# Kernel tuning notes

Hardware: AMD Instinct MI355X
Metric: run time of the kernel (lower is better)

## Reference

```python
import jax, jax.numpy as jnp
import numpy as np

EPS = 1e-5

def _bn(x, gamma, beta):
    # BatchNorm1d forward (batch statistics, biased variance) over node dim
    mu = x.mean(axis=0)
    var = x.var(axis=0)
    return gamma * (x - mu) * jax.lax.rsqrt(var + EPS) + beta

def _gcn_conv(x, W, b, src, dst, n):
    # PyG GCNConv: h = x @ W; symmetric norm with self-loops; scatter-add to dst
    h = x @ W                                   # [N, out]
    ones = jnp.ones(src.shape, dtype=h.dtype)
    deg = jax.ops.segment_sum(ones, dst, num_segments=n) + 1.0  # +1 self-loop
    dinv = jax.lax.rsqrt(deg)                   # deg >= 1 always
    norm = dinv[src] * dinv[dst]                # [E]
    agg = jax.ops.segment_sum(h[src] * norm[:, None], dst, num_segments=n)
    agg = agg + h * (dinv * dinv)[:, None]      # self-loop contribution
    return agg + b

def setup_inputs() -> dict:
    key = jax.random.key(0)
    ks = jax.random.split(key, 10)
    N, E = 100000, 1600000
    Din, Dh, Dout = 256, 128, 128
    e_prev = jax.random.normal(ks[0], (N, Din), dtype=jnp.float32)
    edge_index = jax.random.randint(ks[1], (2, E), 0, N, dtype=jnp.int64)
    proj_W = jax.random.normal(ks[2], (Din, Din), dtype=jnp.float32) * 0.02
    proj_b = jnp.zeros((Din,), dtype=jnp.float32)
    W1 = jax.random.normal(ks[3], (Din, Dh), dtype=jnp.float32) * 0.05
    b1 = jnp.zeros((Dh,), dtype=jnp.float32)
    gamma1 = jnp.ones((Dh,), dtype=jnp.float32)
    beta1 = jnp.zeros((Dh,), dtype=jnp.float32)
    W2 = jax.random.normal(ks[4], (Dh, Dout), dtype=jnp.float32) * 0.05
    b2 = jnp.zeros((Dout,), dtype=jnp.float32)
    gamma2 = jnp.ones((Dout,), dtype=jnp.float32)
    beta2 = jnp.zeros((Dout,), dtype=jnp.float32)
    return {"e_prev": e_prev, "edge_index": edge_index,
            "proj_W": proj_W, "proj_b": proj_b,
            "W1": W1, "b1": b1, "gamma1": gamma1, "beta1": beta1,
            "W2": W2, "b2": b2, "gamma2": gamma2, "beta2": beta2}

def reference(e_prev, edge_index, proj_W, proj_b, W1, b1, gamma1, beta1, W2, b2, gamma2, beta2):
    n = e_prev.shape[0]
    src, dst = edge_index[0], edge_index[1]
    # input_projection (input_dim != hidden_dim branch)
    x = e_prev @ proj_W + proj_b
    x = _gcn_conv(x, W1, b1, src, dst, n)
    x = _bn(x, gamma1, beta1)
    x = jax.nn.relu(x)
    # dropout(0.2) is identity in eval mode
    x = _gcn_conv(x, W2, b2, src, dst, n)
    x = _bn(x, gamma2, beta2)
    return x
```

## Files before the change

kernel.cpp:

```cpp
#include <hip/hip_runtime.h>
#include <hip/hip_bf16.h>
#include <math.h>

#define BN_EPS 1e-5f
#define CAP 6144
#define MAXB 512

typedef __attribute__((ext_vector_type(8))) short short8;
typedef __attribute__((ext_vector_type(4))) float floatx4;

__device__ inline float4 ntload4(const float* p) {
    floatx4 v = __builtin_nontemporal_load((const floatx4*)p);
    return make_float4(v.x, v.y, v.z, v.w);
}

__global__ __launch_bounds__(128) void prep_kernel(
    const float* __restrict__ PW, const float* __restrict__ W1,
    const float* __restrict__ pb, const float* __restrict__ W2,
    __hip_bfloat16* __restrict__ Wf1, __hip_bfloat16* __restrict__ Wf2,
    float* __restrict__ bc, int* __restrict__ bcursor, int nb)
{
    int bid = blockIdx.x;
    int tid = threadIdx.x;
    if (bid < 256) {
        int k = bid, c = tid;
        float acc = 0.f;
        for (int kk = 0; kk < 256; ++kk) acc = fmaf(PW[k * 256 + kk], W1[kk * 128 + c], acc);
        int kc = k >> 5, r5 = k & 31, qq = r5 >> 3, j = r5 & 7;
        int ct = c >> 4, l16 = c & 15;
        int lane = qq * 16 + l16;
        Wf1[(((kc * 8 + ct) * 64) + lane) * 8 + j] = __float2bfloat16(acc);
    } else if (bid == 256) {
        int c = tid;
        float acc = 0.f;
        for (int k = 0; k < 256; ++k) acc = fmaf(pb[k], W1[k * 128 + c], acc);
        bc[c] = acc;
    } else if (bid < 385) {
        int t = (bid - 257) * 128 + tid;
        int j    = t & 7;
        int lane = (t >> 3) & 63;
        int ct   = (t >> 9) & 7;
        int kc   = t >> 12;
        int k = kc * 32 + ((lane >> 4) & 3) * 8 + j;
        int c = ct * 16 + (lane & 15);
        Wf2[t] = __float2bfloat16(W2[k * 128 + c]);
    } else {
        int i = (bid - 385) * 128 + tid;
        if (i < nb) bcursor[i] = i * CAP;
        if (bid == 385 && tid < 2) bcursor[nb + 8 + tid] = 0;
    }
}

__global__ __launch_bounds__(256) void bucket_kernel(
    const int* __restrict__ src, const int* __restrict__ dst,
    int* __restrict__ bcursor, unsigned* __restrict__ buck, int E, int nb)
{
    __shared__ int h[MAXB], resv[MAXB], cur[MAXB];
    for (int t = threadIdx.x; t < nb; t += 256) { h[t] = 0; cur[t] = 0; }
    __syncthreads();
    int per = (E + gridDim.x - 1) / gridDim.x;
    int e0 = blockIdx.x * per;
    int e1 = min(e0 + per, E);
    for (int e = e0 + threadIdx.x; e < e1; e += 256) {
        int d = __builtin_nontemporal_load(&dst[e]);
        atomicAdd(&h[d >> 8], 1);
    }
    __syncthreads();
    for (int t = threadIdx.x; t < nb; t += 256) {
        int c = h[t];
        if (c > 0) resv[t] = atomicAdd(&bcursor[t], c);
    }
    __syncthreads();
    for (int e = e0 + threadIdx.x; e < e1; e += 256) {
        int d = __builtin_nontemporal_load(&dst[e]);
        int s = __builtin_nontemporal_load(&src[e]);
        int b = d >> 8;
        int pos = resv[b] + atomicAdd(&cur[b], 1);
        buck[pos] = ((unsigned)(d & 255) << 17) | (unsigned)s;
    }
}

__global__ __launch_bounds__(256) void csr_kernel(
    const unsigned* __restrict__ buck, const int* __restrict__ bcursor,
    int* __restrict__ cnt, int* __restrict__ rowptr, float* __restrict__ dinv,
    int* __restrict__ ssrc, int N)
{
    __shared__ int h[256], sc[256], lcur[256], redu[256];
    int b = blockIdx.x;
    int t = threadIdx.x;
    int part = 0;
    for (int i = t; i < b; i += 256) part += bcursor[i] - i * CAP;
    redu[t] = part;
    h[t] = 0;
    __syncthreads();
    for (int off = 128; off > 0; off >>= 1) {
        if (t < off) redu[t] += redu[t + off];
        __syncthreads();
    }
    int cb = redu[0];

    int base = b * CAP;
    int nB = bcursor[b] - base;
    for (int i = t; i < nB; i += 256) {
        unsigned v = buck[base + i];
        atomicAdd(&h[v >> 17], 1);
    }
    __syncthreads();
    int myc = h[t];
    sc[t] = myc;
    __syncthreads();
    for (int off = 1; off < 256; off <<= 1) {
        int x = (t >= off) ? sc[t - off] : 0;
        __syncthreads();
        sc[t] += x;
        __syncthreads();
    }
    int ex = sc[t] - myc;
    lcur[t] = ex;
    int node = b * 256 + t;
    if (node < N) {
        cnt[node]    = myc;
        rowptr[node] = cb + ex;
        dinv[node]   = rsqrtf((float)myc + 1.0f);
    }
    __syncthreads();
    for (int i = t; i < nB; i += 256) {
        unsigned v = buck[base + i];
        int dloc = v >> 17;
        int pos = cb + atomicAdd(&lcur[dloc], 1);
        ssrc[pos] = (int)(v & 0x1FFFFu);
    }
}

__device__ inline short8 cvt8(float4 a, float4 b) {
    __hip_bfloat162 p0 = __float22bfloat162_rn(make_float2(a.x, a.y));
    __hip_bfloat162 p1 = __float22bfloat162_rn(make_float2(a.z, a.w));
    __hip_bfloat162 p2 = __float22bfloat162_rn(make_float2(b.x, b.y));
    __hip_bfloat162 p3 = __float22bfloat162_rn(make_float2(b.z, b.w));
    union { short8 s; __hip_bfloat162 h[4]; } u;
    u.h[0] = p0; u.h[1] = p1; u.h[2] = p2; u.h[3] = p3;
    return u.s;
}

template <int K, bool BN>
__global__ __launch_bounds__(256) void mfma_gemm(
    const float* __restrict__ X, const short* __restrict__ Wf,
    const float* __restrict__ bias, const float* __restrict__ dinv,
    const float* __restrict__ scale, const float* __restrict__ shift,
    __hip_bfloat16* __restrict__ Hs, int N)
{
    const int wave = threadIdx.x >> 6;
    const int lane = threadIdx.x & 63;
    const int l16  = lane & 15;
    const int q    = lane >> 4;
    const int r0   = blockIdx.x * 128 + wave * 32;

    const int ra0 = min(r0 + l16, N - 1);
    const int ra1 = min(r0 + 16 + l16, N - 1);
    const float* pA0 = X + (size_t)ra0 * K + q * 8;
    const float* pA1 = X + (size_t)ra1 * K + q * 8;
    const short8* WF = (const short8*)Wf;

    floatx4 acc[2][8];
#pragma unroll
    for (int rt = 0; rt < 2; ++rt)
#pragma unroll
        for (int ct = 0; ct < 8; ++ct) { acc[rt][ct][0] = 0.f; acc[rt][ct][1] = 0.f; acc[rt][ct][2] = 0.f; acc[rt][ct][3] = 0.f; }

#pragma unroll
    for (int kc = 0; kc < K / 32; ++kc) {
        short8 b[8];
#pragma unroll
        for (int ct = 0; ct < 8; ++ct) b[ct] = WF[(kc * 8 + ct) * 64 + lane];

        float4 x00 = ntload4(pA0 + kc * 32);
        float4 x01 = ntload4(pA0 + kc * 32 + 4);
        float4 x10 = ntload4(pA1 + kc * 32);
        float4 x11 = ntload4(pA1 + kc * 32 + 4);
        if (BN) {
            float4 sc0 = *(const float4*)(scale + kc * 32 + q * 8);
            float4 sc1 = *(const float4*)(scale + kc * 32 + q * 8 + 4);
            float4 sh0 = *(const float4*)(shift + kc * 32 + q * 8);
            float4 sh1 = *(const float4*)(shift + kc * 32 + q * 8 + 4);
            x00.x = fmaxf(fmaf(x00.x, sc0.x, sh0.x), 0.f);
            x00.y = fmaxf(fmaf(x00.y, sc0.y, sh0.y), 0.f);
            x00.z = fmaxf(fmaf(x00.z, sc0.z, sh0.z), 0.f);
            x00.w = fmaxf(fmaf(x00.w, sc0.w, sh0.w), 0.f);
            x01.x = fmaxf(fmaf(x01.x, sc1.x, sh1.x), 0.f);
            x01.y = fmaxf(fmaf(x01.y, sc1.y, sh1.y), 0.f);
            x01.z = fmaxf(fmaf(x01.z, sc1.z, sh1.z), 0.f);
            x01.w = fmaxf(fmaf(x01.w, sc1.w, sh1.w), 0.f);
            x10.x = fmaxf(fmaf(x10.x, sc0.x, sh0.x), 0.f);
            x10.y = fmaxf(fmaf(x10.y, sc0.y, sh0.y), 0.f);
            x10.z = fmaxf(fmaf(x10.z, sc0.z, sh0.z), 0.f);
            x10.w = fmaxf(fmaf(x10.w, sc0.w, sh0.w), 0.f);
            x11.x = fmaxf(fmaf(x11.x, sc1.x, sh1.x), 0.f);
            x11.y = fmaxf(fmaf(x11.y, sc1.y, sh1.y), 0.f);
            x11.z = fmaxf(fmaf(x11.z, sc1.z, sh1.z), 0.f);
            x11.w = fmaxf(fmaf(x11.w, sc1.w, sh1.w), 0.f);
        }
        short8 a0 = cvt8(x00, x01);
        short8 a1 = cvt8(x10, x11);
#pragma unroll
        for (int ct = 0; ct < 8; ++ct) {
            acc[0][ct] = __builtin_amdgcn_mfma_f32_16x16x32_bf16(a0, b[ct], acc[0][ct], 0, 0, 0);
            acc[1][ct] = __builtin_amdgcn_mfma_f32_16x16x32_bf16(a1, b[ct], acc[1][ct], 0, 0, 0);
        }
    }

    float bb[8];
#pragma unroll
    for (int ct = 0; ct < 8; ++ct) bb[ct] = bias ? bias[ct * 16 + l16] : 0.f;

#pragma unroll
    for (int rt = 0; rt < 2; ++rt) {
        int rbase = r0 + rt * 16 + q * 4;
        float dv[4];
#pragma unroll
        for (int i = 0; i < 4; ++i) dv[i] = dinv[min(rbase + i, N - 1)];
#pragma unroll
        for (int ct = 0; ct < 8; ++ct) {
#pragma unroll
            for (int i = 0; i < 4; ++i) {
                int row = rbase + i;
                if (row < N)
                    Hs[(size_t)row * 128 + ct * 16 + l16] =
                        __float2bfloat16((acc[rt][ct][i] + bb[ct]) * dv[i]);
            }
        }
    }
}

__device__ inline void accrow(uint4 u, float* a) {
    a[0] += __uint_as_float(u.x << 16);
    a[1] += __uint_as_float(u.x & 0xffff0000u);
    a[2] += __uint_as_float(u.y << 16);
    a[3] += __uint_as_float(u.y & 0xffff0000u);
    a[4] += __uint_as_float(u.z << 16);
    a[5] += __uint_as_float(u.z & 0xffff0000u);
    a[6] += __uint_as_float(u.w << 16);
    a[7] += __uint_as_float(u.w & 0xffff0000u);
}

__global__ __launch_bounds__(256) void agg_gather_kernel(
    const uint4* __restrict__ Hq, const int* __restrict__ rowptr,
    const int* __restrict__ cnt, const int* __restrict__ ssrc,
    const float* __restrict__ dinv, const float* __restrict__ bias,
    float* __restrict__ Out, int node0, int N)
{
    int node = node0 + blockIdx.x * 4 + (threadIdx.x >> 6);
    if (node >= N) return;
    int lane = threadIdx.x & 63;
    int q    = lane >> 4;
    int l16  = lane & 15;

    float a0[8] = {0,0,0,0,0,0,0,0};
    float a1[8] = {0,0,0,0,0,0,0,0};
    float a2[8] = {0,0,0,0,0,0,0,0};
    float a3[8] = {0,0,0,0,0,0,0,0};

    if (q == 0) accrow(Hq[(size_t)node * 16 + l16], a0);

    int start = rowptr[node];
    int num   = cnt[node];
    int j = 0;
    for (; j + 16 <= num; j += 16) {
        int e = start + j + q;
        int s0 = ssrc[e];
        int s1 = ssrc[e + 4];
        int s2 = ssrc[e + 8];
        int s3 = ssrc[e + 12];
        uint4 u0 = Hq[(size_t)s0 * 16 + l16];
        uint4 u1 = Hq[(size_t)s1 * 16 + l16];
        uint4 u2 = Hq[(size_t)s2 * 16 + l16];
        uint4 u3 = Hq[(size_t)s3 * 16 + l16];
        accrow(u0, a0);
        accrow(u1, a1);
        accrow(u2, a2);
        accrow(u3, a3);
    }
    for (; j + 4 <= num; j += 4) {
        int s = ssrc[start + j + q];
        accrow(Hq[(size_t)s * 16 + l16], a0);
    }
    int rem = num - j;
    if (q < rem) {
        int s = ssrc[start + j + q];
        accrow(Hq[(size_t)s * 16 + l16], a1);
    }

#pragma unroll
    for (int i = 0; i < 8; ++i) {
        float v = a0[i] + a1[i] + a2[i] + a3[i];
        v += __shfl_xor(v, 16, 64);
        v += __shfl_xor(v, 32, 64);
        a0[i] = v;
    }

    if (q == 0) {
        float di = dinv[node];
        const float4* B4 = (const float4*)bias;
        float4 bb0 = B4[l16 * 2];
        float4 bb1 = B4[l16 * 2 + 1];
        float4 o0, o1;
        o0.x = fmaf(a0[0], di, bb0.x);
        o0.y = fmaf(a0[1], di, bb0.y);
        o0.z = fmaf(a0[2], di, bb0.z);
        o0.w = fmaf(a0[3], di, bb0.w);
        o1.x = fmaf(a0[4], di, bb1.x);
        o1.y = fmaf(a0[5], di, bb1.y);
        o1.z = fmaf(a0[6], di, bb1.z);
        o1.w = fmaf(a0[7], di, bb1.w);
        float4* O4 = (float4*)(Out + (size_t)node * 128 + l16 * 8);
        O4[0] = o0;
        O4[1] = o1;
    }
}

__global__ __launch_bounds__(256) void bn_stats_kernel(
    const float* __restrict__ A, float* __restrict__ partS, float* __restrict__ partQ,
    int N, int R,
    const float* __restrict__ gamma, const float* __restrict__ beta,
    float* __restrict__ scale, float* __restrict__ shift, int* __restrict__ ctr)
{
    int col4   = threadIdx.x & 31;
    int rowoff = threadIdx.x >> 5;
    int r0 = blockIdx.x * R;
    int r1 = min(r0 + R, N);
    float4 s = make_float4(0.f, 0.f, 0.f, 0.f);
    float4 qq = make_float4(0.f, 0.f, 0.f, 0.f);
#pragma unroll 4
    for (int r = r0 + rowoff; r < r1; r += 8) {
        float4 v = *(const float4*)&A[(size_t)r * 128 + col4 * 4];
        s.x += v.x; s.y += v.y; s.z += v.z; s.w += v.w;
        qq.x = fmaf(v.x, v.x, qq.x);
        qq.y = fmaf(v.y, v.y, qq.y);
        qq.z = fmaf(v.z, v.z, qq.z);
        qq.w = fmaf(v.w, v.w, qq.w);
    }
    __shared__ float4 ls[256], lq[256];
    ls[threadIdx.x] = s;
    lq[threadIdx.x] = qq;
    __syncthreads();
    if (threadIdx.x < 32) {
        float4 ts = ls[threadIdx.x], tq = lq[threadIdx.x];
#pragma unroll
        for (int k = 1; k < 8; ++k) {
            float4 xs = ls[k * 32 + threadIdx.x];
            float4 xq = lq[k * 32 + threadIdx.x];
            ts.x += xs.x; ts.y += xs.y; ts.z += xs.z; ts.w += xs.w;
            tq.x += xq.x; tq.y += xq.y; tq.z += xq.z; tq.w += xq.w;
        }
        *(float4*)&partS[(size_t)blockIdx.x * 128 + threadIdx.x * 4] = ts;
        *(float4*)&partQ[(size_t)blockIdx.x * 128 + threadIdx.x * 4] = tq;
    }
    __syncthreads();
    __shared__ int amLast;
    if (threadIdx.x == 0) {
        __threadfence();
        amLast = (atomicAdd(ctr, 1) == (int)gridDim.x - 1);
    }
    __syncthreads();
    if (!amLast) return;
    __threadfence();
    int c = threadIdx.x & 127;
    int h = threadIdx.x >> 7;
    float fs = 0.f, fq = 0.f;
    for (int b = h * 128; b < h * 128 + 128; ++b) {
        fs += partS[(size_t)b * 128 + c];
        fq += partQ[(size_t)b * 128 + c];
    }
    __shared__ float rs_[256], rq_[256];
    rs_[threadIdx.x] = fs;
    rq_[threadIdx.x] = fq;
    __syncthreads();
    if (threadIdx.x < 128) {
        float S = rs_[threadIdx.x] + rs_[threadIdx.x + 128];
        float Q = rq_[threadIdx.x] + rq_[threadIdx.x + 128];
        float m = S / (float)N;
        float v = Q / (float)N - m * m;
        float rs = rsqrtf(v + BN_EPS);
        float sc = gamma[c] * rs;
        scale[c] = sc;
        shift[c] = fmaf(-m, sc, beta[c]);
    }
}

__global__ void bn_apply_kernel(float* __restrict__ A, const float* __restrict__ scale,
                                const float* __restrict__ shift, int N) {
    int i = blockIdx.x * blockDim.x + threadIdx.x;
    if (i >= N * 32) return;
    int c4 = i & 31;
    float4 v  = ((float4*)A)[i];
    float4 sc = ((const float4*)scale)[c4];
    float4 sh = ((const float4*)shift)[c4];
    v.x = fmaf(v.x, sc.x, sh.x);
    v.y = fmaf(v.y, sc.y, sh.y);
    v.z = fmaf(v.z, sc.z, sh.z);
    v.w = fmaf(v.w, sc.w, sh.w);
    ((float4*)A)[i] = v;
}

extern "C" void kernel_launch(void* const* d_in, const int* in_sizes, int n_in,
                              void* d_out, int out_size, void* d_ws, size_t ws_size,
                              hipStream_t stream) {
    const float* e_prev = (const float*)d_in[0];
    const int*   edges  = (const int*)d_in[1];
    const float* proj_W = (const float*)d_in[2];
    const float* proj_b = (const float*)d_in[3];
    const float* W1     = (const float*)d_in[4];
    const float* b1     = (const float*)d_in[5];
    const float* gamma1 = (const float*)d_in[6];
    const float* beta1  = (const float*)d_in[7];
    const float* W2     = (const float*)d_in[8];
    const float* b2     = (const float*)d_in[9];
    const float* gamma2 = (const float*)d_in[10];
    const float* beta2  = (const float*)d_in[11];
    float* out = (float*)d_out;

    const int N = in_sizes[0] / 256;
    const int E = in_sizes[1] / 2;
    const int* src = edges;
    const int* dst = edges + E;
    const int nb = (N + 255) >> 8;
    const int R = (N + 255) / 256;

    char* p = (char*)d_ws;
    const size_t NH = (size_t)N * 128;
    __hip_bfloat16* Hs = (__hip_bfloat16*)p;  p += NH * 2;
    unsigned* buck  = (unsigned*)p; p += (size_t)nb * CAP * 4;
    int* ssrc   = (int*)p;  p += (size_t)E * 4;
    int* cnt    = (int*)p;  p += (size_t)N * 4;
    int* rowptr = (int*)p;  p += (size_t)N * 4;
    float* dinv = (float*)p; p += (size_t)N * 4;
    int* bcursor = (int*)p; p += (size_t)(nb + 16) * 4;
    float* bc   = (float*)p; p += 128 * 4;
    float* stats = (float*)p; p += 1536 * 4;
    float* partS = (float*)p; p += 256 * 128 * 4;
    float* partQ = (float*)p; p += 256 * 128 * 4;
    __hip_bfloat16* Wf1 = (__hip_bfloat16*)p; p += 256 * 128 * 2;
    __hip_bfloat16* Wf2 = (__hip_bfloat16*)p; p += 128 * 128 * 2;
    float* scale1 = stats, *shift1 = stats + 128;
    float* scale2 = stats + 256, *shift2 = stats + 384;
    int* ctr1 = bcursor + nb + 8;
    int* ctr2 = bcursor + nb + 9;

    prep_kernel<<<389, 128, 0, stream>>>(proj_W, W1, proj_b, W2, Wf1, Wf2, bc, bcursor, nb);
    bucket_kernel<<<512, 256, 0, stream>>>(src, dst, bcursor, buck, E, nb);
    csr_kernel<<<nb, 256, 0, stream>>>(buck, bcursor, cnt, rowptr, dinv, ssrc, N);

    const int gemm_grid = (N + 127) / 128;
    const int Nh = ((N / 2) + 3) & ~3;
    const int g1 = Nh / 4;
    const int g2 = (N - Nh + 3) / 4;

    mfma_gemm<256, false><<<gemm_grid, 256, 0, stream>>>(
        e_prev, (const short*)Wf1, bc, dinv, nullptr, nullptr, Hs, N);
    agg_gather_kernel<<<g1, 256, 0, stream>>>(
        (const uint4*)Hs, rowptr, cnt, ssrc, dinv, b1, out, 0, N);
    agg_gather_kernel<<<g2, 256, 0, stream>>>(
        (const uint4*)Hs, rowptr, cnt, ssrc, dinv, b1, out, Nh, N);
    bn_stats_kernel<<<256, 256, 0, stream>>>(out, partS, partQ, N, R,
                                             gamma1, beta1, scale1, shift1, ctr1);

    mfma_gemm<128, true><<<gemm_grid, 256, 0, stream>>>(
        out, (const short*)Wf2, nullptr, dinv, scale1, shift1, Hs, N);
    agg_gather_kernel<<<g1, 256, 0, stream>>>(
        (const uint4*)Hs, rowptr, cnt, ssrc, dinv, b2, out, 0, N);
    agg_gather_kernel<<<g2, 256, 0, stream>>>(
        (const uint4*)Hs, rowptr, cnt, ssrc, dinv, b2, out, Nh, N);
    bn_stats_kernel<<<256, 256, 0, stream>>>(out, partS, partQ, N, R,
                                             gamma2, beta2, scale2, shift2, ctr2);
    bn_apply_kernel<<<(N * 32 + 255) / 256, 256, 0, stream>>>(out, scale2, shift2, N);
}
```

Before: 571.9 us.

## Fuse GEMM1 with bucketing, move dinv scaling into gather, fuse final BN

Several separate changes. GEMM1 now runs in one launch alongside edge bucketing, so the dense work overlaps the scatter. Because GEMM1 no longer needs dinv from the CSR pass, the source-side dinv scaling moves into the gather loop as an extra per-edge load. The split two-launch aggregation becomes a single launch, and the final BN stats and apply are merged into one kernel that uses a grid-wide spin barrier. The prep matmul loops also get four independent accumulators; the costs are extra dinv gathers per edge and a spin barrier that assumes all 256 blocks are resident at once.

New measurement: 596.5 us. 4.3% more time.

```diff
diff --git a/kernel.cpp b/kernel.cpp
--- a/kernel.cpp
+++ b/kernel.cpp
@@ -24,17 +24,28 @@
     int tid = threadIdx.x;
     if (bid < 256) {
         int k = bid, c = tid;
-        float acc = 0.f;
-        for (int kk = 0; kk < 256; ++kk) acc = fmaf(PW[k * 256 + kk], W1[kk * 128 + c], acc);
+        float a0 = 0.f, a1 = 0.f, a2 = 0.f, a3 = 0.f;
+        for (int kk = 0; kk < 256; kk += 4) {
+            a0 = fmaf(PW[k * 256 + kk],     W1[(kk)     * 128 + c], a0);
+            a1 = fmaf(PW[k * 256 + kk + 1], W1[(kk + 1) * 128 + c], a1);
+            a2 = fmaf(PW[k * 256 + kk + 2], W1[(kk + 2) * 128 + c], a2);
+            a3 = fmaf(PW[k * 256 + kk + 3], W1[(kk + 3) * 128 + c], a3);
+        }
+        float acc = (a0 + a1) + (a2 + a3);
         int kc = k >> 5, r5 = k & 31, qq = r5 >> 3, j = r5 & 7;
         int ct = c >> 4, l16 = c & 15;
         int lane = qq * 16 + l16;
         Wf1[(((kc * 8 + ct) * 64) + lane) * 8 + j] = __float2bfloat16(acc);
     } else if (bid == 256) {
         int c = tid;
-        float acc = 0.f;
-        for (int k = 0; k < 256; ++k) acc = fmaf(pb[k], W1[k * 128 + c], acc);
-        bc[c] = acc;
+        float a0 = 0.f, a1 = 0.f, a2 = 0.f, a3 = 0.f;
+        for (int k = 0; k < 256; k += 4) {
+            a0 = fmaf(pb[k],     W1[(k)     * 128 + c], a0);
+            a1 = fmaf(pb[k + 1], W1[(k + 1) * 128 + c], a1);
+            a2 = fmaf(pb[k + 2], W1[(k + 2) * 128 + c], a2);
+            a3 = fmaf(pb[k + 3], W1[(k + 3) * 128 + c], a3);
+        }
+        bc[c] = (a0 + a1) + (a2 + a3);
     } else if (bid < 385) {
         int t = (bid - 257) * 128 + tid;
         int j    = t & 7;
@@ -51,15 +62,16 @@
     }
 }
 
-__global__ __launch_bounds__(256) void bucket_kernel(
+__device__ void bucket_body(
     const int* __restrict__ src, const int* __restrict__ dst,
-    int* __restrict__ bcursor, unsigned* __restrict__ buck, int E, int nb)
+    int* __restrict__ bcursor, unsigned* __restrict__ buck,
+    int E, int nb, int nblocks, int bid)
 {
     __shared__ int h[MAXB], resv[MAXB], cur[MAXB];
     for (int t = threadIdx.x; t < nb; t += 256) { h[t] = 0; cur[t] = 0; }
     __syncthreads();
-    int per = (E + gridDim.x - 1) / gridDim.x;
-    int e0 = blockIdx.x * per;
+    int per = (E + nblocks - 1) / nblocks;
+    int e0 = bid * per;
     int e1 = min(e0 + per, E);
     for (int e = e0 + threadIdx.x; e < e1; e += 256) {
         int d = __builtin_nontemporal_load(&dst[e]);
@@ -143,9 +155,10 @@
 }
 
 template <int K, bool BN>
-__global__ __launch_bounds__(256) void mfma_gemm(
+__device__ void gemm_body(
+    int bid,
     const float* __restrict__ X, const short* __restrict__ Wf,
-    const float* __restrict__ bias, const float* __restrict__ dinv,
+    const float* __restrict__ bias,
     const float* __restrict__ scale, const float* __restrict__ shift,
     __hip_bfloat16* __restrict__ Hs, int N)
 {
@@ -153,7 +166,7 @@
     const int lane = threadIdx.x & 63;
     const int l16  = lane & 15;
     const int q    = lane >> 4;
-    const int r0   = blockIdx.x * 128 + wave * 32;
+    const int r0   = bid * 128 + wave * 32;
 
     const int ra0 = min(r0 + l16, N - 1);
     const int ra1 = min(r0 + 16 + l16, N - 1);
@@ -215,9 +228,6 @@
 #pragma unroll
     for (int rt = 0; rt < 2; ++rt) {
         int rbase = r0 + rt * 16 + q * 4;
-        float dv[4];
-#pragma unroll
-        for (int i = 0; i < 4; ++i) dv[i] = dinv[min(rbase + i, N - 1)];
 #pragma unroll
         for (int ct = 0; ct < 8; ++ct) {
 #pragma unroll
@@ -225,30 +235,53 @@
                 int row = rbase + i;
                 if (row < N)
                     Hs[(size_t)row * 128 + ct * 16 + l16] =
-                        __float2bfloat16((acc[rt][ct][i] + bb[ct]) * dv[i]);
+                        __float2bfloat16(acc[rt][ct][i] + bb[ct]);
             }
         }
     }
 }
 
-__device__ inline void accrow(uint4 u, float* a) {
-    a[0] += __uint_as_float(u.x << 16);
-    a[1] += __uint_as_float(u.x & 0xffff0000u);
-    a[2] += __uint_as_float(u.y << 16);
-    a[3] += __uint_as_float(u.y & 0xffff0000u);
-    a[4] += __uint_as_float(u.z << 16);
-    a[5] += __uint_as_float(u.z & 0xffff0000u);
-    a[6] += __uint_as_float(u.w << 16);
-    a[7] += __uint_as_float(u.w & 0xffff0000u);
+__global__ __launch_bounds__(256) void gemm1_bucket_kernel(
+    const float* __restrict__ X, const short* __restrict__ Wf,
+    const float* __restrict__ bias,
+    __hip_bfloat16* __restrict__ Hs, int N, int gemmGrid,
+    const int* __restrict__ src, const int* __restrict__ dst,
+    int* __restrict__ bcursor, unsigned* __restrict__ buck, int E, int nb,
+    int bucketGrid)
+{
+    if ((int)blockIdx.x < gemmGrid)
+        gemm_body<256, false>(blockIdx.x, X, Wf, bias, nullptr, nullptr, Hs, N);
+    else
+        bucket_body(src, dst, bcursor, buck, E, nb, bucketGrid,
+                    (int)blockIdx.x - gemmGrid);
+}
+
+__global__ __launch_bounds__(256) void mfma_gemm2_kernel(
+    const float* __restrict__ X, const short* __restrict__ Wf,
+    const float* __restrict__ scale, const float* __restrict__ shift,
+    __hip_bfloat16* __restrict__ Hs, int N)
+{
+    gemm_body<128, true>(blockIdx.x, X, Wf, nullptr, scale, shift, Hs, N);
+}
+
+__device__ inline void accrow(uint4 u, float d, float* a) {
+    a[0] = fmaf(__uint_as_float(u.x << 16),         d, a[0]);
+    a[1] = fmaf(__uint_as_float(u.x & 0xffff0000u), d, a[1]);
+    a[2] = fmaf(__uint_as_float(u.y << 16),         d, a[2]);
+    a[3] = fmaf(__uint_as_float(u.y & 0xffff0000u), d, a[3]);
+    a[4] = fmaf(__uint_as_float(u.z << 16),         d, a[4]);
+    a[5] = fmaf(__uint_as_float(u.z & 0xffff0000u), d, a[5]);
+    a[6] = fmaf(__uint_as_float(u.w << 16),         d, a[6]);
+    a[7] = fmaf(__uint_as_float(u.w & 0xffff0000u), d, a[7]);
 }
 
 __global__ __launch_bounds__(256) void agg_gather_kernel(
     const uint4* __restrict__ Hq, const int* __restrict__ rowptr,
     const int* __restrict__ cnt, const int* __restrict__ ssrc,
     const float* __restrict__ dinv, const float* __restrict__ bias,
-    float* __restrict__ Out, int node0, int N)
-{
-    int node = node0 + blockIdx.x * 4 + (threadIdx.x >> 6);
+    float* __restrict__ Out, int N)
+{
+    int node = blockIdx.x * 4 + (threadIdx.x >> 6);
     if (node >= N) return;
     int lane = threadIdx.x & 63;
     int q    = lane >> 4;
@@ -259,7 +292,8 @@
     float a2[8] = {0,0,0,0,0,0,0,0};
     float a3[8] = {0,0,0,0,0,0,0,0};
 
-    if (q == 0) accrow(Hq[(size_t)node * 16 + l16], a0);
+    float di = dinv[node];
+    if (q == 0) accrow(Hq[(size_t)node * 16 + l16], di, a0);
 
     int start = rowptr[node];
     int num   = cnt[node];
@@ -270,23 +304,27 @@
         int s1 = ssrc[e + 4];
         int s2 = ssrc[e + 8];
         int s3 = ssrc[e + 12];
+        float d0 = dinv[s0];
+        float d1 = dinv[s1];
+        float d2 = dinv[s2];
+        float d3 = dinv[s3];
         uint4 u0 = Hq[(size_t)s0 * 16 + l16];
         uint4 u1 = Hq[(size_t)s1 * 16 + l16];
         uint4 u2 = Hq[(size_t)s2 * 16 + l16];
         uint4 u3 = Hq[(size_t)s3 * 16 + l16];
-        accrow(u0, a0);
-        accrow(u1, a1);
-        accrow(u2, a2);
-        accrow(u3, a3);
+        accrow(u0, d0, a0);
+        accrow(u1, d1, a1);
+        accrow(u2, d2, a2);
+        accrow(u3, d3, a3);
     }
     for (; j + 4 <= num; j += 4) {
         int s = ssrc[start + j + q];
-        accrow(Hq[(size_t)s * 16 + l16], a0);
+        accrow(Hq[(size_t)s * 16 + l16], dinv[s], a0);
     }
     int rem = num - j;
     if (q < rem) {
         int s = ssrc[start + j + q];
-        accrow(Hq[(size_t)s * 16 + l16], a1);
+        accrow(Hq[(size_t)s * 16 + l16], dinv[s], a1);
     }
 
 #pragma unroll
@@ -298,7 +336,6 @@
     }
 
     if (q == 0) {
-        float di = dinv[node];
         const float4* B4 = (const float4*)bias;
         float4 bb0 = B4[l16 * 2];
         float4 bb1 = B4[l16 * 2 + 1];
@@ -386,19 +423,83 @@
     }
 }
 
-__global__ void bn_apply_kernel(float* __restrict__ A, const float* __restrict__ scale,
-                                const float* __restrict__ shift, int N) {
-    int i = blockIdx.x * blockDim.x + threadIdx.x;
-    if (i >= N * 32) return;
-    int c4 = i & 31;
-    float4 v  = ((float4*)A)[i];
-    float4 sc = ((const float4*)scale)[c4];
-    float4 sh = ((const float4*)shift)[c4];
-    v.x = fmaf(v.x, sc.x, sh.x);
-    v.y = fmaf(v.y, sc.y, sh.y);
-    v.z = fmaf(v.z, sc.z, sh.z);
-    v.w = fmaf(v.w, sc.w, sh.w);
-    ((float4*)A)[i] = v;
+__global__ __launch_bounds__(256) void bn_stats_apply_kernel(
+    float* __restrict__ A, float* __restrict__ partS, float* __restrict__ partQ,
+    int N, int R,
+    const float* __restrict__ gamma, const float* __restrict__ beta,
+    int* __restrict__ ctr)
+{
+    int col4   = threadIdx.x & 31;
+    int rowoff = threadIdx.x >> 5;
+    int r0 = blockIdx.x * R;
+    int r1 = min(r0 + R, N);
+    float4 s = make_float4(0.f, 0.f, 0.f, 0.f);
+    float4 qq = make_float4(0.f, 0.f, 0.f, 0.f);
+#pragma unroll 4
+    for (int r = r0 + rowoff; r < r1; r += 8) {
+        float4 v = *(const float4*)&A[(size_t)r * 128 + col4 * 4];
+        s.x += v.x; s.y += v.y; s.z += v.z; s.w += v.w;
+        qq.x = fmaf(v.x, v.x, qq.x);
+        qq.y = fmaf(v.y, v.y, qq.y);
+        qq.z = fmaf(v.z, v.z, qq.z);
+        qq.w = fmaf(v.w, v.w, qq.w);
+    }
+    __shared__ float4 ls[256], lq[256];
+    ls[threadIdx.x] = s;
+    lq[threadIdx.x] = qq;
+    __syncthreads();
+    if (threadIdx.x < 32) {
+        float4 ts = ls[threadIdx.x], tq = lq[threadIdx.x];
+#pragma unroll
+        for (int k = 1; k < 8; ++k) {
+            float4 xs = ls[k * 32 + threadIdx.x];
+            float4 xq = lq[k * 32 + threadIdx.x];
+            ts.x += xs.x; ts.y += xs.y; ts.z += xs.z; ts.w += xs.w;
+            tq.x += xq.x; tq.y += xq.y; tq.z += xq.z; tq.w += xq.w;
+        }
+        *(float4*)&partS[(size_t)blockIdx.x * 128 + threadIdx.x * 4] = ts;
+        *(float4*)&partQ[(size_t)blockIdx.x * 128 + threadIdx.x * 4] = tq;
+    }
+    __syncthreads();
+    if (threadIdx.x == 0) {
+        __threadfence();
+        atomicAdd(ctr, 1);
+        while (atomicAdd(ctr, 0) < (int)gridDim.x) { }
+    }
+    __syncthreads();
+    __threadfence();
+    int c = threadIdx.x & 127;
+    int h = threadIdx.x >> 7;
+    float fs = 0.f, fq = 0.f;
+    for (int b = h * 128; b < h * 128 + 128; ++b) {
+        fs += partS[(size_t)b * 128 + c];
+        fq += partQ[(size_t)b * 128 + c];
+    }
+    __shared__ float rs_[256], rq_[256];
+    __shared__ float s_sc[128], s_sh[128];
+    rs_[threadIdx.x] = fs;
+    rq_[threadIdx.x] = fq;
+    __syncthreads();
+    if (threadIdx.x < 128) {
+        float S = rs_[threadIdx.x] + rs_[threadIdx.x + 128];
+        float Q = rq_[threadIdx.x] + rq_[threadIdx.x + 128];
+        float m = S / (float)N;
+        float v = Q / (float)N - m * m;
+        float rs = rsqrtf(v + BN_EPS);
+        float sc = gamma[threadIdx.x] * rs;
+        s_sc[threadIdx.x] = sc;
+        s_sh[threadIdx.x] = fmaf(-m, sc, beta[threadIdx.x]);
+    }
+    __syncthreads();
+    for (int r = r0 + rowoff; r < r1; r += 8) {
+        float4* pv = (float4*)&A[(size_t)r * 128 + col4 * 4];
+        float4 v = *pv;
+        v.x = fmaf(v.x, s_sc[col4 * 4 + 0], s_sh[col4 * 4 + 0]);
+        v.y = fmaf(v.y, s_sc[col4 * 4 + 1], s_sh[col4 * 4 + 1]);
+        v.z = fmaf(v.z, s_sc[col4 * 4 + 2], s_sh[col4 * 4 + 2]);
+        v.w = fmaf(v.w, s_sc[col4 * 4 + 3], s_sh[col4 * 4 + 3]);
+        *pv = v;
+    }
 }
 
 extern "C" void kernel_launch(void* const* d_in, const int* in_sizes, int n_in,
@@ -441,35 +542,25 @@
     __hip_bfloat16* Wf1 = (__hip_bfloat16*)p; p += 256 * 128 * 2;
     __hip_bfloat16* Wf2 = (__hip_bfloat16*)p; p += 128 * 128 * 2;
     float* scale1 = stats, *shift1 = stats + 128;
-    float* scale2 = stats + 256, *shift2 = stats + 384;
     int* ctr1 = bcursor + nb + 8;
     int* ctr2 = bcursor + nb + 9;
 
+    const int gemm_grid = (N + 127) / 128;
+    const int bucket_grid = 512;
+
     prep_kernel<<<389, 128, 0, stream>>>(proj_W, W1, proj_b, W2, Wf1, Wf2, bc, bcursor, nb);
-    bucket_kernel<<<512, 256, 0, stream>>>(src, dst, bcursor, buck, E, nb);
+    gemm1_bucket_kernel<<<gemm_grid + bucket_grid, 256, 0, stream>>>(
+        e_prev, (const short*)Wf1, bc, Hs, N, gemm_grid,
+        src, dst, bcursor, buck, E, nb, bucket_grid);
     csr_kernel<<<nb, 256, 0, stream>>>(buck, bcursor, cnt, rowptr, dinv, ssrc, N);
-
-    const int gemm_grid = (N + 127) / 128;
-    const int Nh = ((N / 2) + 3) & ~3;
-    const int g1 = Nh / 4;
-    const int g2 = (N - Nh + 3) / 4;
-
-    mfma_gemm<256, false><<<gemm_grid, 256, 0, stream>>>(
-        e_prev, (const short*)Wf1, bc, dinv, nullptr, nullptr, Hs, N);
-    agg_gather_kernel<<<g1, 256, 0, stream>>>(
-        (const uint4*)Hs, rowptr, cnt, ssrc, dinv, b1, out, 0, N);
-    agg_gather_kernel<<<g2, 256, 0, stream>>>(
-        (const uint4*)Hs, rowptr, cnt, ssrc, dinv, b1, out, Nh, N);
+    agg_gather_kernel<<<(N + 3) / 4, 256, 0, stream>>>(
+        (const uint4*)Hs, rowptr, cnt, ssrc, dinv, b1, out, N);
     bn_stats_kernel<<<256, 256, 0, stream>>>(out, partS, partQ, N, R,
                                              gamma1, beta1, scale1, shift1, ctr1);
-
-    mfma_gemm<128, true><<<gemm_grid, 256, 0, stream>>>(
-        out, (const short*)Wf2, nullptr, dinv, scale1, shift1, Hs, N);
-    agg_gather_kernel<<<g1, 256, 0, stream>>>(
-        (const uint4*)Hs, rowptr, cnt, ssrc, dinv, b2, out, 0, N);
-    agg_gather_kernel<<<g2, 256, 0, stream>>>(
-        (const uint4*)Hs, rowptr, cnt, ssrc, dinv, b2, out, Nh, N);
-    bn_stats_kernel<<<256, 256, 0, stream>>>(out, partS, partQ, N, R,
-                                             gamma2, beta2, scale2, shift2, ctr2);
-    bn_apply_kernel<<<(N * 32 + 255) / 256, 256, 0, stream>>>(out, scale2, shift2, N);
-}
+    mfma_gemm2_kernel<<<gemm_grid, 256, 0, stream>>>(
+        out, (const short*)Wf2, scale1, shift1, Hs, N);
+    agg_gather_kernel<<<(N + 3) / 4, 256, 0, stream>>>(
+        (const uint4*)Hs, rowptr, cnt, ssrc, dinv, b2, out, N);
+    bn_stats_apply_kernel<<<256, 256, 0, stream>>>(out, partS, partQ, N, R,
+                                                   gamma2, beta2, ctr2);
+}
```
